# Optimization experiments

Measured on AMD Instinct MI355X. Metric: run time of the kernel, lower is better.

## Reference

```python
import jax, jax.numpy as jnp
import numpy as np

N_STREAMS = 4
N_EMBD = 1024
SINKHORN_ITERS = 10
B, T = 4, 2048


def rmsnorm(x):
    eps = jnp.finfo(x.dtype).eps
    return x * jax.lax.rsqrt(jnp.mean(x * x, axis=-1, keepdims=True) + eps)


def sinkhorn(logits):
    # logits: (B, T, N, N)
    m = jnp.exp(jnp.clip(logits, -20.0, 20.0))
    for _ in range(SINKHORN_ITERS):
        m = m / jnp.maximum(m.sum(axis=-2, keepdims=True), 1e-12)  # column normalize
        m = m / jnp.maximum(m.sum(axis=-1, keepdims=True), 1e-12)  # row normalize
    return m


def setup_inputs() -> dict:
    key = jax.random.key(0)
    k1, k2, k3, k4 = jax.random.split(key, 4)
    state = jax.random.normal(k1, (B, T, N_STREAMS, N_EMBD), dtype=jnp.float32)
    residual = jax.random.normal(k2, (B, T, N_EMBD), dtype=jnp.float32)
    input_dim = N_STREAMS * N_EMBD
    coeff_dim = N_STREAMS * N_STREAMS + 2 * N_STREAMS
    bound = (3.0 ** 0.5) * (input_dim ** -0.5) * 0.1  # dynamic_init_scale = 0.1
    W = jax.random.uniform(k3, (coeff_dim, input_dim), minval=-bound, maxval=bound, dtype=jnp.float32)
    alpha = jnp.ones((3,), dtype=jnp.float32)
    # bias initialized as in init_weights (residual_init_strength = 4.0)
    pre_value = min(max(1.0 / N_STREAMS, 1e-4), 1.0 - 1e-4)
    pre_bias = float(np.log(pre_value / (1.0 - pre_value)))
    res_bias = np.full((N_STREAMS, N_STREAMS), -4.0, dtype=np.float32)
    np.fill_diagonal(res_bias, 4.0)
    bias = jnp.concatenate([
        jnp.full((N_STREAMS,), pre_bias, dtype=jnp.float32),
        jnp.zeros((N_STREAMS,), dtype=jnp.float32),
        jnp.asarray(res_bias.reshape(-1)),
    ])
    return {"state": state, "residual": residual, "W": W, "alpha": alpha, "bias": bias}


def reference(state, residual, W, alpha, bias):
    N = N_STREAMS
    Bb, Tt, _, D = state.shape
    flat = state.reshape(Bb, Tt, N * D)
    raw = jnp.einsum('btk,ck->btc', rmsnorm(flat).astype(jnp.float32), W.astype(jnp.float32))
    pre_raw, post_raw, res_raw = raw[..., :N], raw[..., N:2 * N], raw[..., 2 * N:]
    pre_b, post_b, res_b = bias[:N], bias[N:2 * N], bias[2 * N:]
    h_pre = jax.nn.sigmoid(alpha[0] * pre_raw + pre_b)                    # (B,T,N)
    h_post = 2.0 * jax.nn.sigmoid(alpha[1] * post_raw + post_b)           # (B,T,N)
    h_res = sinkhorn((alpha[2] * res_raw + res_b).reshape(Bb, Tt, N, N))  # (B,T,N,N)
    pre = jnp.einsum('btn,btnd->btd', h_pre.astype(state.dtype), state)
    mixed = jnp.einsum('btij,btjd->btid', h_res.astype(state.dtype), state)
    new_state = mixed + h_post.astype(state.dtype)[..., None] * residual[:, :, None, :]
    return pre, new_state
```

## Files before the change

### kernel.cpp

```cpp
#include <hip/hip_runtime.h>
#include <hip/hip_bf16.h>
#include <math.h>

#define NSTR 4
#define DEMB 1024
#define KDIM 4096
#define CTOT 24
#define NTOK 8192
#define EPSF 1.1920928955078125e-07f

typedef __attribute__((ext_vector_type(8))) short short8;
typedef __attribute__((ext_vector_type(4))) float f32x4;

__device__ __forceinline__ short8 pack8(float4 a, float4 b) {
    union { short8 s; __hip_bfloat162 h[4]; } u;
    u.h[0] = __float22bfloat162_rn(float2{a.x, a.y});
    u.h[1] = __float22bfloat162_rn(float2{a.z, a.w});
    u.h[2] = __float22bfloat162_rn(float2{b.x, b.y});
    u.h[3] = __float22bfloat162_rn(float2{b.z, b.w});
    return u.s;
}

__global__ __launch_bounds__(256, 2) void k_rawgate(
    const float* __restrict__ state,
    const float* __restrict__ W,
    const float* __restrict__ alpha,
    const float* __restrict__ bias,
    float* __restrict__ out)
{
    const int tid = threadIdx.x;
    const int w = tid >> 6, lane = tid & 63, q = lane >> 4, mn = lane & 15;
    const int tok0 = blockIdx.x * 16;
    const int k0 = w * 1024 + q * 8;

    const float* Ap  = state + (size_t)(tok0 + mn) * KDIM + k0;
    const float* Bp0 = W + (size_t)mn * KDIM + k0;
    int r1 = 16 + mn; if (r1 > 23) r1 = 23;
    const float* Bp1 = W + (size_t)r1 * KDIM + k0;

    f32x4 acc0 = {0.f, 0.f, 0.f, 0.f};
    f32x4 acc1 = {0.f, 0.f, 0.f, 0.f};
    float ss = 0.f;

#pragma unroll 2
    for (int s = 0; s < 32; ++s) {
        const int off = s * 32;
        const float4 a0  = *(const float4*)(Ap + off);
        const float4 a1  = *(const float4*)(Ap + off + 4);
        const float4 b00 = *(const float4*)(Bp0 + off);
        const float4 b01 = *(const float4*)(Bp0 + off + 4);
        const float4 b10 = *(const float4*)(Bp1 + off);
        const float4 b11 = *(const float4*)(Bp1 + off + 4);
        ss += a0.x*a0.x + a0.y*a0.y + a0.z*a0.z + a0.w*a0.w
            + a1.x*a1.x + a1.y*a1.y + a1.z*a1.z + a1.w*a1.w;
        const short8 af  = pack8(a0, a1);
        const short8 bf0 = pack8(b00, b01);
        const short8 bf1 = pack8(b10, b11);
        acc0 = __builtin_amdgcn_mfma_f32_16x16x32_bf16(af, bf0, acc0, 0, 0, 0);
        acc1 = __builtin_amdgcn_mfma_f32_16x16x32_bf16(af, bf1, acc1, 0, 0, 0);
    }

    __shared__ float part[4][16][28];
    __shared__ float ssb[4][4][16];
#pragma unroll
    for (int r = 0; r < 4; ++r) part[w][q * 4 + r][mn] = acc0[r];
    if (mn < 8) {
#pragma unroll
        for (int r = 0; r < 4; ++r) part[w][q * 4 + r][16 + mn] = acc1[r];
    }
    ssb[w][q][mn] = ss;
    __syncthreads();

    if (tid < 16) {
        const int t = tid;
        float r[24];
#pragma unroll
        for (int c = 0; c < 24; ++c)
            r[c] = part[0][t][c] + part[1][t][c] + part[2][t][c] + part[3][t][c];
        float sssum = 0.f;
#pragma unroll
        for (int ww = 0; ww < 4; ++ww)
#pragma unroll
            for (int qq = 0; qq < 4; ++qq) sssum += ssb[ww][qq][t];

        const float scale = rsqrtf(sssum * (1.f / KDIM) + EPSF);
        const float a0 = alpha[0], a1 = alpha[1], a2 = alpha[2];
        float h[24];
#pragma unroll
        for (int n = 0; n < 4; ++n) {
            float x = a0 * (r[n] * scale) + bias[n];
            h[n] = 1.f / (1.f + __expf(-x));
        }
#pragma unroll
        for (int n = 0; n < 4; ++n) {
            float x = a1 * (r[4 + n] * scale) + bias[4 + n];
            h[4 + n] = 2.f / (1.f + __expf(-x));
        }
        float m[16];
#pragma unroll
        for (int e = 0; e < 16; ++e) {
            float x = a2 * (r[8 + e] * scale) + bias[8 + e];
            x = fminf(fmaxf(x, -20.f), 20.f);
            m[e] = __expf(x);
        }
#pragma unroll
        for (int it = 0; it < 10; ++it) {
#pragma unroll
            for (int jj = 0; jj < 4; ++jj) {
                float cs = m[jj] + m[4 + jj] + m[8 + jj] + m[12 + jj];
                float inv = __builtin_amdgcn_rcpf(fmaxf(cs, 1e-12f));
                m[jj] *= inv; m[4 + jj] *= inv; m[8 + jj] *= inv; m[12 + jj] *= inv;
            }
#pragma unroll
            for (int ii = 0; ii < 4; ++ii) {
                float rs = m[4*ii] + m[4*ii+1] + m[4*ii+2] + m[4*ii+3];
                float inv = __builtin_amdgcn_rcpf(fmaxf(rs, 1e-12f));
                m[4*ii] *= inv; m[4*ii+1] *= inv; m[4*ii+2] *= inv; m[4*ii+3] *= inv;
            }
        }
#pragma unroll
        for (int e = 0; e < 16; ++e) h[8 + e] = m[e];

        float* hp = out + (size_t)NTOK * DEMB + (size_t)(tok0 + t) * KDIM;
#pragma unroll
        for (int c = 0; c < 24; ++c) hp[c] = h[c];
    }
}

__global__ __launch_bounds__(256) void k_mix(
    const float* __restrict__ state,
    const float* __restrict__ residual,
    float* out)
{
    const int token = blockIdx.x;
    const int tid = threadIdx.x;
    const float* hh = out + (size_t)NTOK * DEMB + (size_t)token * KDIM;
    float h[24];
#pragma unroll
    for (int c = 0; c < 24; ++c) h[c] = hh[c];
    __syncthreads();

    const float4* sp = (const float4*)(state + (size_t)token * KDIM);
    const float4 x0 = sp[tid];
    const float4 x1 = sp[256 + tid];
    const float4 x2 = sp[512 + tid];
    const float4 x3 = sp[768 + tid];
    const float4 rr = ((const float4*)(residual + (size_t)token * DEMB))[tid];

    const float hp0 = h[0], hp1 = h[1], hp2 = h[2], hp3 = h[3];
    float4 pre;
    pre.x = hp0*x0.x + hp1*x1.x + hp2*x2.x + hp3*x3.x;
    pre.y = hp0*x0.y + hp1*x1.y + hp2*x2.y + hp3*x3.y;
    pre.z = hp0*x0.z + hp1*x1.z + hp2*x2.z + hp3*x3.z;
    pre.w = hp0*x0.w + hp1*x1.w + hp2*x2.w + hp3*x3.w;
    ((float4*)(out + (size_t)token * DEMB))[tid] = pre;

    float4* ns = (float4*)(out + (size_t)NTOK * DEMB + (size_t)token * KDIM);
#pragma unroll
    for (int i2 = 0; i2 < 4; ++i2) {
        const float w0 = h[8 + 4*i2 + 0];
        const float w1 = h[8 + 4*i2 + 1];
        const float w2 = h[8 + 4*i2 + 2];
        const float w3 = h[8 + 4*i2 + 3];
        const float hp = h[4 + i2];
        float4 o;
        o.x = w0*x0.x + w1*x1.x + w2*x2.x + w3*x3.x + hp*rr.x;
        o.y = w0*x0.y + w1*x1.y + w2*x2.y + w3*x3.y + hp*rr.y;
        o.z = w0*x0.z + w1*x1.z + w2*x2.z + w3*x3.z + hp*rr.z;
        o.w = w0*x0.w + w1*x1.w + w2*x2.w + w3*x3.w + hp*rr.w;
        ns[i2 * 256 + tid] = o;
    }
}

extern "C" void kernel_launch(void* const* d_in, const int* in_sizes, int n_in,
                              void* d_out, int out_size, void* d_ws, size_t ws_size,
                              hipStream_t stream) {
    const float* state    = (const float*)d_in[0];
    const float* residual = (const float*)d_in[1];
    const float* W        = (const float*)d_in[2];
    const float* alpha    = (const float*)d_in[3];
    const float* bias     = (const float*)d_in[4];
    float* out = (float*)d_out;

    hipLaunchKernelGGL(k_rawgate, dim3(NTOK / 16), dim3(256), 0, stream,
                       state, W, alpha, bias, out);
    hipLaunchKernelGGL(k_mix, dim3(NTOK), dim3(256), 0, stream,
                       state, residual, out);
}
```

Measured before the change: 319.9 us.

## Fuse gate computation and stream mixing into a single kernel

Merges the gating/sinkhorn kernel with the mixing kernel, so each 16-token block keeps its 24 coefficients in LDS and then applies them to its own tokens, with each wave handling four tokens. This removes the second launch and the global round-trip of the coefficients through the output buffer. The state is re-read right after the GEMM pass, so it may hit in cache. The trade-off is a less parallel mix phase: 512 blocks each loop over four tokens instead of 8192 single-token blocks, which can lower memory-level parallelism.

```diff
diff --git a/kernel.cpp b/kernel.cpp
--- a/kernel.cpp
+++ b/kernel.cpp
@@ -21,8 +21,9 @@
     return u.s;
 }
 
-__global__ __launch_bounds__(256, 2) void k_rawgate(
+__global__ __launch_bounds__(256, 2) void k_fused(
     const float* __restrict__ state,
+    const float* __restrict__ residual,
     const float* __restrict__ W,
     const float* __restrict__ alpha,
     const float* __restrict__ bias,
@@ -62,6 +63,7 @@
 
     __shared__ float part[4][16][28];
     __shared__ float ssb[4][4][16];
+    __shared__ float h_lds[16][24];
 #pragma unroll
     for (int r = 0; r < 4; ++r) part[w][q * 4 + r][mn] = acc0[r];
     if (mn < 8) {
@@ -85,16 +87,15 @@
 
         const float scale = rsqrtf(sssum * (1.f / KDIM) + EPSF);
         const float a0 = alpha[0], a1 = alpha[1], a2 = alpha[2];
-        float h[24];
 #pragma unroll
         for (int n = 0; n < 4; ++n) {
             float x = a0 * (r[n] * scale) + bias[n];
-            h[n] = 1.f / (1.f + __expf(-x));
+            h_lds[t][n] = 1.f / (1.f + __expf(-x));
         }
 #pragma unroll
         for (int n = 0; n < 4; ++n) {
             float x = a1 * (r[4 + n] * scale) + bias[4 + n];
-            h[4 + n] = 2.f / (1.f + __expf(-x));
+            h_lds[t][4 + n] = 2.f / (1.f + __expf(-x));
         }
         float m[16];
 #pragma unroll
@@ -119,56 +120,71 @@
             }
         }
 #pragma unroll
-        for (int e = 0; e < 16; ++e) h[8 + e] = m[e];
-
-        float* hp = out + (size_t)NTOK * DEMB + (size_t)(tok0 + t) * KDIM;
-#pragma unroll
-        for (int c = 0; c < 24; ++c) hp[c] = h[c];
-    }
-}
-
-__global__ __launch_bounds__(256) void k_mix(
-    const float* __restrict__ state,
-    const float* __restrict__ residual,
-    float* out)
-{
-    const int token = blockIdx.x;
-    const int tid = threadIdx.x;
-    const float* hh = out + (size_t)NTOK * DEMB + (size_t)token * KDIM;
-    float h[24];
-#pragma unroll
-    for (int c = 0; c < 24; ++c) h[c] = hh[c];
+        for (int e = 0; e < 16; ++e) h_lds[t][8 + e] = m[e];
+    }
     __syncthreads();
 
-    const float4* sp = (const float4*)(state + (size_t)token * KDIM);
-    const float4 x0 = sp[tid];
-    const float4 x1 = sp[256 + tid];
-    const float4 x2 = sp[512 + tid];
-    const float4 x3 = sp[768 + tid];
-    const float4 rr = ((const float4*)(residual + (size_t)token * DEMB))[tid];
-
-    const float hp0 = h[0], hp1 = h[1], hp2 = h[2], hp3 = h[3];
-    float4 pre;
-    pre.x = hp0*x0.x + hp1*x1.x + hp2*x2.x + hp3*x3.x;
-    pre.y = hp0*x0.y + hp1*x1.y + hp2*x2.y + hp3*x3.y;
-    pre.z = hp0*x0.z + hp1*x1.z + hp2*x2.z + hp3*x3.z;
-    pre.w = hp0*x0.w + hp1*x1.w + hp2*x2.w + hp3*x3.w;
-    ((float4*)(out + (size_t)token * DEMB))[tid] = pre;
-
-    float4* ns = (float4*)(out + (size_t)NTOK * DEMB + (size_t)token * KDIM);
-#pragma unroll
-    for (int i2 = 0; i2 < 4; ++i2) {
-        const float w0 = h[8 + 4*i2 + 0];
-        const float w1 = h[8 + 4*i2 + 1];
-        const float w2 = h[8 + 4*i2 + 2];
-        const float w3 = h[8 + 4*i2 + 3];
-        const float hp = h[4 + i2];
-        float4 o;
-        o.x = w0*x0.x + w1*x1.x + w2*x2.x + w3*x3.x + hp*rr.x;
-        o.y = w0*x0.y + w1*x1.y + w2*x2.y + w3*x3.y + hp*rr.y;
-        o.z = w0*x0.z + w1*x1.z + w2*x2.z + w3*x3.z + hp*rr.z;
-        o.w = w0*x0.w + w1*x1.w + w2*x2.w + w3*x3.w + hp*rr.w;
-        ns[i2 * 256 + tid] = o;
+#pragma unroll 1
+    for (int tt = 0; tt < 4; ++tt) {
+        const int t = w * 4 + tt;
+        const int token = tok0 + t;
+
+        const float4 h03 = *(const float4*)&h_lds[t][0];
+        const float4 h47 = *(const float4*)&h_lds[t][4];
+        const float4 hr0 = *(const float4*)&h_lds[t][8];
+        const float4 hr1 = *(const float4*)&h_lds[t][12];
+        const float4 hr2 = *(const float4*)&h_lds[t][16];
+        const float4 hr3 = *(const float4*)&h_lds[t][20];
+
+        const float4* sp = (const float4*)(state + (size_t)token * KDIM);
+        const float4* rp = (const float4*)(residual + (size_t)token * DEMB);
+        float4* pre_p = (float4*)(out + (size_t)token * DEMB);
+        float4* ns_p  = (float4*)(out + (size_t)NTOK * DEMB + (size_t)token * KDIM);
+
+#pragma unroll
+        for (int dc = 0; dc < 4; ++dc) {
+            const int idx = dc * 64 + lane;
+            const float4 x0 = sp[idx];
+            const float4 x1 = sp[256 + idx];
+            const float4 x2 = sp[512 + idx];
+            const float4 x3 = sp[768 + idx];
+            const float4 rr = rp[idx];
+
+            float4 pre;
+            pre.x = h03.x*x0.x + h03.y*x1.x + h03.z*x2.x + h03.w*x3.x;
+            pre.y = h03.x*x0.y + h03.y*x1.y + h03.z*x2.y + h03.w*x3.y;
+            pre.z = h03.x*x0.z + h03.y*x1.z + h03.z*x2.z + h03.w*x3.z;
+            pre.w = h03.x*x0.w + h03.y*x1.w + h03.z*x2.w + h03.w*x3.w;
+            pre_p[idx] = pre;
+
+            float4 o0;
+            o0.x = hr0.x*x0.x + hr0.y*x1.x + hr0.z*x2.x + hr0.w*x3.x + h47.x*rr.x;
+            o0.y = hr0.x*x0.y + hr0.y*x1.y + hr0.z*x2.y + hr0.w*x3.y + h47.x*rr.y;
+            o0.z = hr0.x*x0.z + hr0.y*x1.z + hr0.z*x2.z + hr0.w*x3.z + h47.x*rr.z;
+            o0.w = hr0.x*x0.w + hr0.y*x1.w + hr0.z*x2.w + hr0.w*x3.w + h47.x*rr.w;
+            ns_p[idx] = o0;
+
+            float4 o1;
+            o1.x = hr1.x*x0.x + hr1.y*x1.x + hr1.z*x2.x + hr1.w*x3.x + h47.y*rr.x;
+            o1.y = hr1.x*x0.y + hr1.y*x1.y + hr1.z*x2.y + hr1.w*x3.y + h47.y*rr.y;
+            o1.z = hr1.x*x0.z + hr1.y*x1.z + hr1.z*x2.z + hr1.w*x3.z + h47.y*rr.z;
+            o1.w = hr1.x*x0.w + hr1.y*x1.w + hr1.z*x2.w + hr1.w*x3.w + h47.y*rr.w;
+            ns_p[256 + idx] = o1;
+
+            float4 o2;
+            o2.x = hr2.x*x0.x + hr2.y*x1.x + hr2.z*x2.x + hr2.w*x3.x + h47.z*rr.x;
+            o2.y = hr2.x*x0.y + hr2.y*x1.y + hr2.z*x2.y + hr2.w*x3.y + h47.z*rr.y;
+            o2.z = hr2.x*x0.z + hr2.y*x1.z + hr2.z*x2.z + hr2.w*x3.z + h47.z*rr.z;
+            o2.w = hr2.x*x0.w + hr2.y*x1.w + hr2.z*x2.w + hr2.w*x3.w + h47.z*rr.w;
+            ns_p[512 + idx] = o2;
+
+            float4 o3;
+            o3.x = hr3.x*x0.x + hr3.y*x1.x + hr3.z*x2.x + hr3.w*x3.x + h47.w*rr.x;
+            o3.y = hr3.x*x0.y + hr3.y*x1.y + hr3.z*x2.y + hr3.w*x3.y + h47.w*rr.y;
+            o3.z = hr3.x*x0.z + hr3.y*x1.z + hr3.z*x2.z + hr3.w*x3.z + h47.w*rr.z;
+            o3.w = hr3.x*x0.w + hr3.y*x1.w + hr3.z*x2.w + hr3.w*x3.w + h47.w*rr.w;
+            ns_p[768 + idx] = o3;
+        }
     }
 }
 
@@ -182,8 +198,6 @@
     const float* bias     = (const float*)d_in[4];
     float* out = (float*)d_out;
 
-    hipLaunchKernelGGL(k_rawgate, dim3(NTOK / 16), dim3(256), 0, stream,
-                       state, W, alpha, bias, out);
-    hipLaunchKernelGGL(k_mix, dim3(NTOK), dim3(256), 0, stream,
-                       state, residual, out);
+    hipLaunchKernelGGL(k_fused, dim3(NTOK / 16), dim3(256), 0, stream,
+                       state, residual, W, alpha, bias, out);
 }
```

New measurement: 321.3 us. Within noise of the previous version (+0.5%).

## Stage state rows through swizzled LDS with coalesced loads and register prefetch

Applied to the files above, without the earlier changes.

The gate GEMM kernel now loads each token's state row with fully coalesced float4 loads into a swizzled shared-memory tile, in chunks of 512 columns. The next chunk is prefetched into registers while the current one is consumed. The block grows to 8 waves, which split K and reduce partials through LDS. This replaces strided per-lane global loads of the A operand, at the cost of two barriers per chunk and 32KB of LDS per block, which may limit occupancy.

```diff
diff --git a/kernel.cpp b/kernel.cpp
--- a/kernel.cpp
+++ b/kernel.cpp
@@ -21,7 +21,7 @@
     return u.s;
 }
 
-__global__ __launch_bounds__(256, 2) void k_rawgate(
+__global__ __launch_bounds__(512, 4) void k_raw(
     const float* __restrict__ state,
     const float* __restrict__ W,
     const float* __restrict__ alpha,
@@ -31,37 +31,70 @@
     const int tid = threadIdx.x;
     const int w = tid >> 6, lane = tid & 63, q = lane >> 4, mn = lane & 15;
     const int tok0 = blockIdx.x * 16;
-    const int k0 = w * 1024 + q * 8;
-
-    const float* Ap  = state + (size_t)(tok0 + mn) * KDIM + k0;
-    const float* Bp0 = W + (size_t)mn * KDIM + k0;
+
+    __shared__ float tile[16 * 512];
+    __shared__ float part[8][16][28];
+    __shared__ float ssb[8][4][16];
+
+    const int t0 = 2 * w, t1 = t0 + 1;
+    const int swz0 = t0 & 7, swz1 = t1 & 7;
+    const int rsw  = mn & 7;
+    const float* src0 = state + (size_t)(tok0 + t0) * KDIM;
+    const float* src1 = state + (size_t)(tok0 + t1) * KDIM;
+
+    const int kq = w * 64 + q * 8;
+    const float* Bp0 = W + (size_t)mn * KDIM + kq;
     int r1 = 16 + mn; if (r1 > 23) r1 = 23;
-    const float* Bp1 = W + (size_t)r1 * KDIM + k0;
+    const float* Bp1 = W + (size_t)r1 * KDIM + kq;
 
     f32x4 acc0 = {0.f, 0.f, 0.f, 0.f};
     f32x4 acc1 = {0.f, 0.f, 0.f, 0.f};
     float ss = 0.f;
 
-#pragma unroll 2
-    for (int s = 0; s < 32; ++s) {
-        const int off = s * 32;
-        const float4 a0  = *(const float4*)(Ap + off);
-        const float4 a1  = *(const float4*)(Ap + off + 4);
-        const float4 b00 = *(const float4*)(Bp0 + off);
-        const float4 b01 = *(const float4*)(Bp0 + off + 4);
-        const float4 b10 = *(const float4*)(Bp1 + off);
-        const float4 b11 = *(const float4*)(Bp1 + off + 4);
-        ss += a0.x*a0.x + a0.y*a0.y + a0.z*a0.z + a0.w*a0.w
-            + a1.x*a1.x + a1.y*a1.y + a1.z*a1.z + a1.w*a1.w;
-        const short8 af  = pack8(a0, a1);
-        const short8 bf0 = pack8(b00, b01);
-        const short8 bf1 = pack8(b10, b11);
-        acc0 = __builtin_amdgcn_mfma_f32_16x16x32_bf16(af, bf0, acc0, 0, 0, 0);
-        acc1 = __builtin_amdgcn_mfma_f32_16x16x32_bf16(af, bf1, acc1, 0, 0, 0);
-    }
-
-    __shared__ float part[4][16][28];
-    __shared__ float ssb[4][4][16];
+    float4 v00 = *(const float4*)(src0 + 4 * lane);
+    float4 v01 = *(const float4*)(src0 + 256 + 4 * lane);
+    float4 v10 = *(const float4*)(src1 + 4 * lane);
+    float4 v11 = *(const float4*)(src1 + 256 + 4 * lane);
+
+#pragma unroll 1
+    for (int kc = 0; kc < 8; ++kc) {
+        float4 n00, n01, n10, n11;
+        if (kc < 7) {
+            const int kb1 = (kc + 1) * 512;
+            n00 = *(const float4*)(src0 + kb1 + 4 * lane);
+            n01 = *(const float4*)(src0 + kb1 + 256 + 4 * lane);
+            n10 = *(const float4*)(src1 + kb1 + 4 * lane);
+            n11 = *(const float4*)(src1 + kb1 + 256 + 4 * lane);
+        }
+        __syncthreads();
+        *(float4*)&tile[t0 * 512 + (((lane     ) ^ swz0) << 2)] = v00;
+        *(float4*)&tile[t0 * 512 + (((lane + 64) ^ swz0) << 2)] = v01;
+        *(float4*)&tile[t1 * 512 + (((lane     ) ^ swz1) << 2)] = v10;
+        *(float4*)&tile[t1 * 512 + (((lane + 64) ^ swz1) << 2)] = v11;
+        __syncthreads();
+
+        const int kb = kc * 512;
+#pragma unroll
+        for (int ks = 0; ks < 2; ++ks) {
+            const int g = w * 16 + ks * 8 + q * 2;
+            const float4 a0 = *(const float4*)&tile[mn * 512 + (((g    ) ^ rsw) << 2)];
+            const float4 a1 = *(const float4*)&tile[mn * 512 + (((g + 1) ^ rsw) << 2)];
+            const int off = kb + ks * 32;
+            const float4 b00 = *(const float4*)(Bp0 + off);
+            const float4 b01 = *(const float4*)(Bp0 + off + 4);
+            const float4 b10 = *(const float4*)(Bp1 + off);
+            const float4 b11 = *(const float4*)(Bp1 + off + 4);
+            ss += a0.x*a0.x + a0.y*a0.y + a0.z*a0.z + a0.w*a0.w
+                + a1.x*a1.x + a1.y*a1.y + a1.z*a1.z + a1.w*a1.w;
+            const short8 af  = pack8(a0, a1);
+            const short8 bf0 = pack8(b00, b01);
+            const short8 bf1 = pack8(b10, b11);
+            acc0 = __builtin_amdgcn_mfma_f32_16x16x32_bf16(af, bf0, acc0, 0, 0, 0);
+            acc1 = __builtin_amdgcn_mfma_f32_16x16x32_bf16(af, bf1, acc1, 0, 0, 0);
+        }
+        v00 = n00; v01 = n01; v10 = n10; v11 = n11;
+    }
+
 #pragma unroll
     for (int r = 0; r < 4; ++r) part[w][q * 4 + r][mn] = acc0[r];
     if (mn < 8) {
@@ -75,11 +108,15 @@
         const int t = tid;
         float r[24];
 #pragma unroll
-        for (int c = 0; c < 24; ++c)
-            r[c] = part[0][t][c] + part[1][t][c] + part[2][t][c] + part[3][t][c];
+        for (int c = 0; c < 24; ++c) {
+            float v = 0.f;
+#pragma unroll
+            for (int ww = 0; ww < 8; ++ww) v += part[ww][t][c];
+            r[c] = v;
+        }
         float sssum = 0.f;
 #pragma unroll
-        for (int ww = 0; ww < 4; ++ww)
+        for (int ww = 0; ww < 8; ++ww)
 #pragma unroll
             for (int qq = 0; qq < 4; ++qq) sssum += ssb[ww][qq][t];
 
@@ -182,7 +219,7 @@
     const float* bias     = (const float*)d_in[4];
     float* out = (float*)d_out;
 
-    hipLaunchKernelGGL(k_rawgate, dim3(NTOK / 16), dim3(256), 0, stream,
+    hipLaunchKernelGGL(k_raw, dim3(NTOK / 16), dim3(512), 0, stream,
                        state, W, alpha, bias, out);
     hipLaunchKernelGGL(k_mix, dim3(NTOK), dim3(256), 0, stream,
                        state, residual, out);
```

After: 313.6 us. Within noise of the previous version (-2.0%).
